# Optimization experiments

Measured on AMD Instinct MI355X. Metric: run time of the kernel, lower is better.

The kernel has to match this reference:

```python
import jax, jax.numpy as jnp
import numpy as np

N_NODES = 100000
N_EDGES = 3200000
NEG_SLOPE = 0.2  # PyG GATConv default


def _gat_conv(x, src, dst, W, a_src, a_dst, b, num_nodes):
    # x: [N, Fin]; src/dst: [E'] (self-loops already appended)
    h = x @ W                                   # [N, Fout]
    alpha_src = h @ a_src                       # [N]
    alpha_dst = h @ a_dst                       # [N]
    e = jax.nn.leaky_relu(alpha_src[src] + alpha_dst[dst], NEG_SLOPE)  # [E']
    # segment softmax over incoming edges of each destination node
    e_max = jax.ops.segment_max(e, dst, num_segments=num_nodes)
    e_exp = jnp.exp(e - e_max[dst])
    denom = jax.ops.segment_sum(e_exp, dst, num_segments=num_nodes)
    alpha = e_exp / (denom[dst] + 1e-16)        # [E']
    out = jax.ops.segment_sum(h[src] * alpha[:, None], dst, num_segments=num_nodes)
    return out + b


def setup_inputs() -> dict:
    key = jax.random.key(0)
    ks = jax.random.split(key, 10)
    x = jax.random.normal(ks[0], (N_NODES, 1), jnp.float32)
    edge_index = jax.random.randint(ks[1], (2, N_EDGES), 0, N_NODES, dtype=jnp.int64)
    s1 = 1.0  # glorot-ish scales
    return {
        "x": x,
        "edge_index": edge_index,
        "W1": jax.random.normal(ks[2], (1, 20), jnp.float32) * s1,
        "a_src1": jax.random.normal(ks[3], (20,), jnp.float32) * 0.3,
        "a_dst1": jax.random.normal(ks[4], (20,), jnp.float32) * 0.3,
        "b1": jnp.zeros((20,), jnp.float32),
        "W2": jax.random.normal(ks[5], (20, 20), jnp.float32) * (1.0 / np.sqrt(20.0)),
        "a_src2": jax.random.normal(ks[6], (20,), jnp.float32) * 0.3,
        "a_dst2": jax.random.normal(ks[7], (20,), jnp.float32) * 0.3,
        "b2": jnp.zeros((20,), jnp.float32),
        "Wl": jax.random.normal(ks[8], (20, 1), jnp.float32) * (1.0 / np.sqrt(20.0)),
        "bl": jnp.zeros((1,), jnp.float32),
    }


def reference(x, edge_index, W1, a_src1, a_dst1, b1, W2, a_src2, a_dst2, b2, Wl, bl):
    n = x.shape[0]
    loop = jnp.arange(n, dtype=edge_index.dtype)
    src = jnp.concatenate([edge_index[0], loop])  # add_self_loops=True
    dst = jnp.concatenate([edge_index[1], loop])
    h = _gat_conv(x, src, dst, W1, a_src1, a_dst1, b1, n)
    h = jax.nn.relu(h)
    h = _gat_conv(h, src, dst, W2, a_src2, a_dst2, b2, n)
    h = jax.nn.relu(h)
    return h @ Wl + bl  # [N, 1]
```

## Files before the change

### kernel.cpp

```cpp
#include <hip/hip_runtime.h>
#include <hip/hip_fp16.h>

#define FDIM 20
#define NSLOPE 0.2f
#define BSHIFT 7
#define BSIZE 128
#define BCAP 4800
#define MAXBUCK 800
#define PGRID 256
#define HSTRIDE 32
#define ABLK 512
#define ITMAX 13
#define CHCAP 12544
#define OFFSTRIDE 132

__device__ __forceinline__ float lrelu(float v) { return v > 0.f ? v : NSLOPE * v; }

__global__ void k_init(const float* __restrict__ x, const float* __restrict__ W1,
                       const float* __restrict__ a_src, const float* __restrict__ a_dst,
                       float2* __restrict__ PX, float* __restrict__ AD,
                       int* __restrict__ gcur, int N)
{
    int i = blockIdx.x * blockDim.x + threadIdx.x;
    if (i < MAXBUCK) gcur[i] = 0;
    if (i >= N) return;
    float cs = 0.f, cd = 0.f;
#pragma unroll
    for (int f = 0; f < FDIM; ++f) { float w = W1[f]; cs += w * a_src[f]; cd += w * a_dst[f]; }
    float xv = x[i];
    PX[i] = make_float2(xv * cs, xv);
    AD[i] = xv * cd;
}

__global__ void __launch_bounds__(1024)
k_part(const int* __restrict__ ei, int E, int nbuck,
       int* __restrict__ gcur, int* __restrict__ slab)
{
    __shared__ int hist[MAXBUCK];
    __shared__ int lofs[MAXBUCK];
    __shared__ int gbase[MAXBUCK];
    __shared__ int sbuf[CHCAP];
    __shared__ unsigned short sbk[CHCAP];
    const int tid = threadIdx.x;
    const int chunk = (E + PGRID - 1) / PGRID;
    const int c0 = blockIdx.x * chunk;
    const int c1 = min(c0 + chunk, E);
    for (int t = tid; t < nbuck; t += 1024) hist[t] = 0;
    __syncthreads();

    int ent[ITMAX], meta[ITMAX];
#pragma unroll
    for (int it = 0; it < ITMAX; ++it) {
        int i = c0 + tid + (it << 10);
        meta[it] = -1;
        if (i < c1) {
            int s = ei[i], d = ei[E + i];
            int b = d >> BSHIFT;
            int lp = atomicAdd(&hist[b], 1);
            ent[it]  = (s << BSHIFT) | (d & (BSIZE - 1));
            meta[it] = (lp << 10) | b;
        }
    }
    __syncthreads();

    int myc = 0;
    if (tid < nbuck) {
        myc = hist[tid];
        lofs[tid] = myc;
        gbase[tid] = myc ? atomicAdd(gcur + tid, myc) : 0;
    }
    __syncthreads();
    for (int o = 1; o < nbuck; o <<= 1) {
        int v = 0;
        if (tid < nbuck && tid >= o) v = lofs[tid - o];
        __syncthreads();
        if (tid < nbuck && tid >= o) lofs[tid] += v;
        __syncthreads();
    }
    if (tid < nbuck) lofs[tid] -= myc;
    __syncthreads();

#pragma unroll
    for (int it = 0; it < ITMAX; ++it) {
        int m = meta[it];
        if (m >= 0) {
            int b  = m & 1023;
            int lp = m >> 10;
            int pos = lofs[b] + lp;
            sbuf[pos] = ent[it];
            sbk[pos]  = (unsigned short)b;
        }
    }
    __syncthreads();

    const int cnt = c1 - c0;
    for (int i = tid; i < cnt; i += 1024) {
        int b  = sbk[i];
        int gp = gbase[b] + (i - lofs[b]);
        if (gp < BCAP) slab[(size_t)b * BCAP + gp] = sbuf[i];
    }
}

__device__ __forceinline__ void sort_bucket(const int* __restrict__ sp, int cnt,
                                            int* __restrict__ sedge,
                                            int* __restrict__ off,
                                            int* __restrict__ cur)
{
    const int tid = threadIdx.x;
    if (tid < BSIZE + 1) off[tid] = 0;
    __syncthreads();
    for (int i = tid; i < cnt; i += blockDim.x)
        atomicAdd(&off[(sp[i] & (BSIZE - 1)) + 1], 1);
    __syncthreads();
    for (int o = 1; o < BSIZE; o <<= 1) {
        int v = 0;
        if (tid < BSIZE && tid + 1 > o) v = off[tid + 1 - o];
        __syncthreads();
        if (tid < BSIZE) off[tid + 1] += v;
        __syncthreads();
    }
    if (tid < BSIZE) cur[tid] = off[tid];
    __syncthreads();
    for (int i = tid; i < cnt; i += blockDim.x) {
        int e = sp[i];
        int pos = atomicAdd(&cur[e & (BSIZE - 1)], 1);
        sedge[pos] = e >> BSHIFT;
    }
    __syncthreads();
}

__global__ void __launch_bounds__(ABLK)
k_agg1(const int* __restrict__ gcur, const int* __restrict__ slab,
       const float2* __restrict__ PX, const float* __restrict__ AD,
       const float* __restrict__ W1, const float* __restrict__ b1,
       const float* __restrict__ W2,
       const float* __restrict__ as2w, const float* __restrict__ ad2w,
       __half* __restrict__ H, float* __restrict__ AD2,
       int* __restrict__ sedge_g, int* __restrict__ off_g, int N)
{
    __shared__ int sedge[BCAP];
    __shared__ int off[BSIZE + 1], cur[BSIZE];
    __shared__ float sAD[BSIZE];
    __shared__ float sW1[FDIM], sb1[FDIM], sW2[FDIM * FDIM], sas[FDIM], sad[FDIM];
    const int tid = threadIdx.x;
    const int b = blockIdx.x;
    const int dbase = b << BSHIFT;
    if (tid < BSIZE) { int d = dbase + tid; sAD[tid] = (d < N) ? AD[d] : 0.f; }
    for (int t = tid; t < FDIM * FDIM; t += ABLK) sW2[t] = W2[t];
    if (tid >= 480 && tid < 480 + FDIM) {
        int k = tid - 480;
        sW1[k] = W1[k]; sb1[k] = b1[k]; sas[k] = as2w[k]; sad[k] = ad2w[k];
    }
    const int cnt = min(gcur[b], BCAP);
    sort_bucket(slab + (size_t)b * BCAP, cnt, sedge, off, cur);

    for (int i = tid; i < cnt; i += ABLK) sedge_g[(size_t)b * BCAP + i] = sedge[i];
    if (tid <= BSIZE) off_g[b * OFFSTRIDE + tid] = off[tid];

    const int dl = tid >> 2, sub = tid & 3;
    const float adv = sAD[dl];
    float den = 0.f, sx = 0.f;
    const int e1 = off[dl + 1];
#pragma unroll 2
    for (int j = off[dl] + sub; j < e1; j += 4) {
        int s = sedge[j];
        float2 p = PX[s];
        float w = __expf(lrelu(p.x + adv));
        den += w; sx += w * p.y;
    }
    den += __shfl_xor(den, 1); den += __shfl_xor(den, 2);
    sx  += __shfl_xor(sx, 1);  sx  += __shfl_xor(sx, 2);
    const int d = dbase + dl;
    if (sub == 0 && d < N) {
        float2 p = PX[d];
        float w = __expf(lrelu(p.x + adv));
        den += w; sx += w * p.y;
        float sv = sx / (den + 1e-16f);
        float tk[FDIM];
#pragma unroll
        for (int k = 0; k < FDIM; ++k) {
            float tv = sv * sW1[k] + sb1[k];
            tk[k] = tv > 0.f ? tv : 0.f;
        }
        float pas = 0.f, pad = 0.f;
        __half2* hrow = (__half2*)(H + (size_t)d * HSTRIDE);
#pragma unroll
        for (int f = 0; f < FDIM; f += 2) {
            float h0 = 0.f, h1 = 0.f;
#pragma unroll
            for (int k = 0; k < FDIM; ++k) {
                h0 += tk[k] * sW2[k * FDIM + f];
                h1 += tk[k] * sW2[k * FDIM + f + 1];
            }
            hrow[f >> 1] = __halves2half2(__float2half(h0), __float2half(h1));
            pas += h0 * sas[f] + h1 * sas[f + 1];
            pad += h0 * sad[f] + h1 * sad[f + 1];
        }
        *(float*)(H + (size_t)d * HSTRIDE + 24) = pas;
        AD2[d] = pad;
    }
}

__global__ void __launch_bounds__(ABLK)
k_agg2(const int* __restrict__ gcur, const int* __restrict__ sedge_g,
       const int* __restrict__ off_g,
       const __half* __restrict__ H, const float* __restrict__ AD2,
       const float* __restrict__ b2, const float* __restrict__ Wl,
       const float* __restrict__ bl,
       float* __restrict__ out, int N)
{
    __shared__ int sedge[BCAP];
    __shared__ int off[BSIZE + 1];
    __shared__ float sAD[BSIZE];
    __shared__ float sb2[FDIM], sWl[FDIM];
    const int tid = threadIdx.x;
    const int b = blockIdx.x;
    const int dbase = b << BSHIFT;
    if (tid < BSIZE) { int d = dbase + tid; sAD[tid] = (d < N) ? AD2[d] : 0.f; }
    if (tid >= 480 && tid < 480 + FDIM) {
        int k = tid - 480;
        sb2[k] = b2[k]; sWl[k] = Wl[k];
    }
    const int cnt = min(gcur[b], BCAP);
    for (int i = tid; i < cnt; i += ABLK) sedge[i] = sedge_g[(size_t)b * BCAP + i];
    if (tid <= BSIZE) off[tid] = off_g[b * OFFSTRIDE + tid];
    __syncthreads();

    const int dl = tid >> 2, sub = tid & 3;
    const int lane3 = (tid & 63) | 3;
    const float adv = sAD[dl];
    float den = 0.f;
    float acc[8];
#pragma unroll
    for (int t = 0; t < 8; ++t) acc[t] = 0.f;
    const int e1 = off[dl + 1];
#pragma unroll 2
    for (int j = off[dl]; j < e1; ++j) {
        int s = sedge[j];
        uint4 q = ((const uint4*)(H + (size_t)s * HSTRIDE))[sub];
        float al = __shfl(__uint_as_float(q.x), lane3);
        float w = __expf(lrelu(al + adv));
        den += w;
        float2 f;
        f = __half22float2(*(__half2*)&q.x); acc[0] += w * f.x; acc[1] += w * f.y;
        f = __half22float2(*(__half2*)&q.y); acc[2] += w * f.x; acc[3] += w * f.y;
        f = __half22float2(*(__half2*)&q.z); acc[4] += w * f.x; acc[5] += w * f.y;
        f = __half22float2(*(__half2*)&q.w); acc[6] += w * f.x; acc[7] += w * f.y;
    }

    const int d = dbase + dl;
    float r = 0.f;
    if (d < N) {
        uint4 q = ((const uint4*)(H + (size_t)d * HSTRIDE))[sub];
        float al = __shfl(__uint_as_float(q.x), lane3);
        float w = __expf(lrelu(al + adv));
        den += w;
        float hv[8];
        float2 f;
        f = __half22float2(*(__half2*)&q.x); hv[0] = f.x; hv[1] = f.y;
        f = __half22float2(*(__half2*)&q.y); hv[2] = f.x; hv[3] = f.y;
        f = __half22float2(*(__half2*)&q.z); hv[4] = f.x; hv[5] = f.y;
        f = __half22float2(*(__half2*)&q.w); hv[6] = f.x; hv[7] = f.y;
        float inv = 1.f / (den + 1e-16f);
        const int base = sub << 3;
        const int nf = (sub < 2) ? 8 : (sub == 2 ? 4 : 0);
#pragma unroll
        for (int t = 0; t < 8; ++t) {
            if (t < nf) {
                float v = (acc[t] + w * hv[t]) * inv + sb2[base + t];
                v = v > 0.f ? v : 0.f;
                r += v * sWl[base + t];
            }
        }
    }
    r += __shfl_xor(r, 1);
    r += __shfl_xor(r, 2);
    if (sub == 0 && d < N) out[d] = r + bl[0];
}

extern "C" void kernel_launch(void* const* d_in, const int* in_sizes, int n_in,
                              void* d_out, int out_size, void* d_ws, size_t ws_size,
                              hipStream_t stream)
{
    const float* x      = (const float*)d_in[0];
    const int*   ei     = (const int*)d_in[1];
    const float* W1     = (const float*)d_in[2];
    const float* a_src1 = (const float*)d_in[3];
    const float* a_dst1 = (const float*)d_in[4];
    const float* b1     = (const float*)d_in[5];
    const float* W2     = (const float*)d_in[6];
    const float* a_src2 = (const float*)d_in[7];
    const float* a_dst2 = (const float*)d_in[8];
    const float* b2     = (const float*)d_in[9];
    const float* Wl     = (const float*)d_in[10];
    const float* bl     = (const float*)d_in[11];
    float* out = (float*)d_out;

    const int N = in_sizes[0];
    const int E = in_sizes[1] / 2;
    const int NBUCK = (N + BSIZE - 1) >> BSHIFT;

    __half* H    = (__half*)d_ws;
    float2* PX   = (float2*)(H + (size_t)N * HSTRIDE);
    float*  AD   = (float*)(PX + N);
    float*  AD2  = AD + N;
    int*  gcur   = (int*)(AD2 + N);
    int*  slab   = gcur + MAXBUCK;
    int*  sedge_g = slab + (size_t)MAXBUCK * BCAP;
    int*  off_g   = sedge_g + (size_t)MAXBUCK * BCAP;

    const int nb_n = (N + 255) / 256;

    k_init<<<nb_n, 256, 0, stream>>>(x, W1, a_src1, a_dst1, PX, AD, gcur, N);
    k_part<<<PGRID, 1024, 0, stream>>>(ei, E, NBUCK, gcur, slab);
    k_agg1<<<NBUCK, ABLK, 0, stream>>>(gcur, slab, PX, AD, W1, b1, W2,
                                       a_src2, a_dst2, H, AD2, sedge_g, off_g, N);
    k_agg2<<<NBUCK, ABLK, 0, stream>>>(gcur, sedge_g, off_g, H, AD2, b2, Wl, bl, out, N);
}
```

Baseline: 181.8 us.

## Fuse both GAT aggregation layers into one persistent kernel with grid barrier

Merges the two aggregation kernels into a single persistent kernel of 512 blocks, each handling up to two buckets. The sorted edge lists, offsets and per-node layer-2 destination scores stay in shared memory across a software grid barrier, so the global sedge/off/AD2 round trip and one launch go away. The sort's block-level Hillis-Steele prefix scan is replaced by a single-wavefront shuffle scan. The grid barrier assumes all 512 blocks are co-resident, and the doubled shared-memory footprint (about 40KB per block) limits occupancy.

```diff
diff --git a/kernel.cpp b/kernel.cpp
--- a/kernel.cpp
+++ b/kernel.cpp
@@ -10,9 +10,9 @@
 #define PGRID 256
 #define HSTRIDE 32
 #define ABLK 512
+#define FGRID 512
 #define ITMAX 13
 #define CHCAP 12544
-#define OFFSTRIDE 132
 
 __device__ __forceinline__ float lrelu(float v) { return v > 0.f ? v : NSLOPE * v; }
 
@@ -22,7 +22,7 @@
                        int* __restrict__ gcur, int N)
 {
     int i = blockIdx.x * blockDim.x + threadIdx.x;
-    if (i < MAXBUCK) gcur[i] = 0;
+    if (i < MAXBUCK + 1) gcur[i] = 0;
     if (i >= N) return;
     float cs = 0.f, cd = 0.f;
 #pragma unroll
@@ -109,19 +109,27 @@
     const int tid = threadIdx.x;
     if (tid < BSIZE + 1) off[tid] = 0;
     __syncthreads();
-    for (int i = tid; i < cnt; i += blockDim.x)
+    for (int i = tid; i < cnt; i += ABLK)
         atomicAdd(&off[(sp[i] & (BSIZE - 1)) + 1], 1);
     __syncthreads();
-    for (int o = 1; o < BSIZE; o <<= 1) {
-        int v = 0;
-        if (tid < BSIZE && tid + 1 > o) v = off[tid + 1 - o];
-        __syncthreads();
-        if (tid < BSIZE) off[tid + 1] += v;
-        __syncthreads();
-    }
-    if (tid < BSIZE) cur[tid] = off[tid];
-    __syncthreads();
-    for (int i = tid; i < cnt; i += blockDim.x) {
+    if (tid < 64) {
+        int a = off[2 * tid + 1];
+        int c = off[2 * tid + 2];
+        int s = a + c;
+#pragma unroll
+        for (int o = 1; o < 64; o <<= 1) {
+            int t = __shfl_up(s, o);
+            if (tid >= o) s += t;
+        }
+        int ex = s - a - c;
+        off[2 * tid]     = ex;
+        off[2 * tid + 1] = ex + a;
+        cur[2 * tid]     = ex;
+        cur[2 * tid + 1] = ex + a;
+        if (tid == 63) off[BSIZE] = s;
+    }
+    __syncthreads();
+    for (int i = tid; i < cnt; i += ABLK) {
         int e = sp[i];
         int pos = atomicAdd(&cur[e & (BSIZE - 1)], 1);
         sedge[pos] = e >> BSHIFT;
@@ -129,153 +137,153 @@
     __syncthreads();
 }
 
-__global__ void __launch_bounds__(ABLK)
-k_agg1(const int* __restrict__ gcur, const int* __restrict__ slab,
-       const float2* __restrict__ PX, const float* __restrict__ AD,
-       const float* __restrict__ W1, const float* __restrict__ b1,
-       const float* __restrict__ W2,
-       const float* __restrict__ as2w, const float* __restrict__ ad2w,
-       __half* __restrict__ H, float* __restrict__ AD2,
-       int* __restrict__ sedge_g, int* __restrict__ off_g, int N)
-{
-    __shared__ int sedge[BCAP];
-    __shared__ int off[BSIZE + 1], cur[BSIZE];
-    __shared__ float sAD[BSIZE];
+__global__ void __launch_bounds__(ABLK, 4)
+k_fused(const int* __restrict__ gcur, const int* __restrict__ slab,
+        const float2* __restrict__ PX, const float* __restrict__ AD,
+        const float* __restrict__ W1, const float* __restrict__ b1,
+        const float* __restrict__ W2,
+        const float* __restrict__ as2w, const float* __restrict__ ad2w,
+        const float* __restrict__ b2, const float* __restrict__ Wl,
+        const float* __restrict__ bl,
+        __half* __restrict__ H, float* __restrict__ out,
+        int* __restrict__ bar, int N, int nbuck)
+{
+    __shared__ int sedge[2][BCAP];
+    __shared__ int off[2][BSIZE + 1];
+    __shared__ int cur[BSIZE];
+    __shared__ float sADv[2][BSIZE];
+    __shared__ float sAD2[2][BSIZE];
     __shared__ float sW1[FDIM], sb1[FDIM], sW2[FDIM * FDIM], sas[FDIM], sad[FDIM];
+    __shared__ float sb2[FDIM], sWl[FDIM];
     const int tid = threadIdx.x;
-    const int b = blockIdx.x;
-    const int dbase = b << BSHIFT;
-    if (tid < BSIZE) { int d = dbase + tid; sAD[tid] = (d < N) ? AD[d] : 0.f; }
+
     for (int t = tid; t < FDIM * FDIM; t += ABLK) sW2[t] = W2[t];
     if (tid >= 480 && tid < 480 + FDIM) {
         int k = tid - 480;
         sW1[k] = W1[k]; sb1[k] = b1[k]; sas[k] = as2w[k]; sad[k] = ad2w[k];
     }
-    const int cnt = min(gcur[b], BCAP);
-    sort_bucket(slab + (size_t)b * BCAP, cnt, sedge, off, cur);
-
-    for (int i = tid; i < cnt; i += ABLK) sedge_g[(size_t)b * BCAP + i] = sedge[i];
-    if (tid <= BSIZE) off_g[b * OFFSTRIDE + tid] = off[tid];
-
-    const int dl = tid >> 2, sub = tid & 3;
-    const float adv = sAD[dl];
-    float den = 0.f, sx = 0.f;
-    const int e1 = off[dl + 1];
+    if (tid >= 448 && tid < 448 + FDIM) {
+        int k = tid - 448;
+        sb2[k] = b2[k]; sWl[k] = Wl[k];
+    }
+
+    for (int h = 0; h < 2; ++h) {
+        const int b = blockIdx.x + (h << 9);
+        if (b >= nbuck) break;
+        const int dbase = b << BSHIFT;
+        if (tid < BSIZE) { int d = dbase + tid; sADv[h][tid] = (d < N) ? AD[d] : 0.f; }
+        const int cnt = min(gcur[b], BCAP);
+        sort_bucket(slab + (size_t)b * BCAP, cnt, sedge[h], off[h], cur);
+
+        const int dl = tid >> 2, sub = tid & 3;
+        const float adv = sADv[h][dl];
+        float den = 0.f, sx = 0.f;
+        const int e1 = off[h][dl + 1];
 #pragma unroll 2
-    for (int j = off[dl] + sub; j < e1; j += 4) {
-        int s = sedge[j];
-        float2 p = PX[s];
-        float w = __expf(lrelu(p.x + adv));
-        den += w; sx += w * p.y;
-    }
-    den += __shfl_xor(den, 1); den += __shfl_xor(den, 2);
-    sx  += __shfl_xor(sx, 1);  sx  += __shfl_xor(sx, 2);
-    const int d = dbase + dl;
-    if (sub == 0 && d < N) {
-        float2 p = PX[d];
-        float w = __expf(lrelu(p.x + adv));
-        den += w; sx += w * p.y;
-        float sv = sx / (den + 1e-16f);
-        float tk[FDIM];
-#pragma unroll
-        for (int k = 0; k < FDIM; ++k) {
-            float tv = sv * sW1[k] + sb1[k];
-            tk[k] = tv > 0.f ? tv : 0.f;
-        }
-        float pas = 0.f, pad = 0.f;
-        __half2* hrow = (__half2*)(H + (size_t)d * HSTRIDE);
-#pragma unroll
-        for (int f = 0; f < FDIM; f += 2) {
-            float h0 = 0.f, h1 = 0.f;
+        for (int j = off[h][dl] + sub; j < e1; j += 4) {
+            int s = sedge[h][j];
+            float2 p = PX[s];
+            float w = __expf(lrelu(p.x + adv));
+            den += w; sx += w * p.y;
+        }
+        den += __shfl_xor(den, 1); den += __shfl_xor(den, 2);
+        sx  += __shfl_xor(sx, 1);  sx  += __shfl_xor(sx, 2);
+        const int d = dbase + dl;
+        if (sub == 0 && d < N) {
+            float2 p = PX[d];
+            float w = __expf(lrelu(p.x + adv));
+            den += w; sx += w * p.y;
+            float sv = sx / (den + 1e-16f);
+            float tk[FDIM];
 #pragma unroll
             for (int k = 0; k < FDIM; ++k) {
-                h0 += tk[k] * sW2[k * FDIM + f];
-                h1 += tk[k] * sW2[k * FDIM + f + 1];
+                float tv = sv * sW1[k] + sb1[k];
+                tk[k] = tv > 0.f ? tv : 0.f;
             }
-            hrow[f >> 1] = __halves2half2(__float2half(h0), __float2half(h1));
-            pas += h0 * sas[f] + h1 * sas[f + 1];
-            pad += h0 * sad[f] + h1 * sad[f + 1];
-        }
-        *(float*)(H + (size_t)d * HSTRIDE + 24) = pas;
-        AD2[d] = pad;
-    }
-}
-
-__global__ void __launch_bounds__(ABLK)
-k_agg2(const int* __restrict__ gcur, const int* __restrict__ sedge_g,
-       const int* __restrict__ off_g,
-       const __half* __restrict__ H, const float* __restrict__ AD2,
-       const float* __restrict__ b2, const float* __restrict__ Wl,
-       const float* __restrict__ bl,
-       float* __restrict__ out, int N)
-{
-    __shared__ int sedge[BCAP];
-    __shared__ int off[BSIZE + 1];
-    __shared__ float sAD[BSIZE];
-    __shared__ float sb2[FDIM], sWl[FDIM];
-    const int tid = threadIdx.x;
-    const int b = blockIdx.x;
-    const int dbase = b << BSHIFT;
-    if (tid < BSIZE) { int d = dbase + tid; sAD[tid] = (d < N) ? AD2[d] : 0.f; }
-    if (tid >= 480 && tid < 480 + FDIM) {
-        int k = tid - 480;
-        sb2[k] = b2[k]; sWl[k] = Wl[k];
-    }
-    const int cnt = min(gcur[b], BCAP);
-    for (int i = tid; i < cnt; i += ABLK) sedge[i] = sedge_g[(size_t)b * BCAP + i];
-    if (tid <= BSIZE) off[tid] = off_g[b * OFFSTRIDE + tid];
-    __syncthreads();
-
-    const int dl = tid >> 2, sub = tid & 3;
-    const int lane3 = (tid & 63) | 3;
-    const float adv = sAD[dl];
-    float den = 0.f;
-    float acc[8];
-#pragma unroll
-    for (int t = 0; t < 8; ++t) acc[t] = 0.f;
-    const int e1 = off[dl + 1];
+            float pas = 0.f, pad = 0.f;
+            __half2* hrow = (__half2*)(H + (size_t)d * HSTRIDE);
+#pragma unroll
+            for (int f = 0; f < FDIM; f += 2) {
+                float h0 = 0.f, h1 = 0.f;
+#pragma unroll
+                for (int k = 0; k < FDIM; ++k) {
+                    h0 += tk[k] * sW2[k * FDIM + f];
+                    h1 += tk[k] * sW2[k * FDIM + f + 1];
+                }
+                hrow[f >> 1] = __halves2half2(__float2half(h0), __float2half(h1));
+                pas += h0 * sas[f] + h1 * sas[f + 1];
+                pad += h0 * sad[f] + h1 * sad[f + 1];
+            }
+            *(float*)(H + (size_t)d * HSTRIDE + 24) = pas;
+            sAD2[h][dl] = pad;
+        }
+    }
+
+    __threadfence();
+    __syncthreads();
+    if (tid == 0) {
+        atomicAdd(bar, 1);
+        while (__hip_atomic_load(bar, __ATOMIC_ACQUIRE, __HIP_MEMORY_SCOPE_AGENT)
+               < (int)gridDim.x)
+            __builtin_amdgcn_s_sleep(2);
+    }
+    __syncthreads();
+    __threadfence();
+
+    for (int h = 0; h < 2; ++h) {
+        const int b = blockIdx.x + (h << 9);
+        if (b >= nbuck) break;
+        const int dbase = b << BSHIFT;
+        const int dl = tid >> 2, sub = tid & 3;
+        const int lane3 = (tid & 63) | 3;
+        const float adv = sAD2[h][dl];
+        float den = 0.f;
+        float acc[8];
+#pragma unroll
+        for (int t = 0; t < 8; ++t) acc[t] = 0.f;
+        const int e1 = off[h][dl + 1];
 #pragma unroll 2
-    for (int j = off[dl]; j < e1; ++j) {
-        int s = sedge[j];
-        uint4 q = ((const uint4*)(H + (size_t)s * HSTRIDE))[sub];
-        float al = __shfl(__uint_as_float(q.x), lane3);
-        float w = __expf(lrelu(al + adv));
-        den += w;
-        float2 f;
-        f = __half22float2(*(__half2*)&q.x); acc[0] += w * f.x; acc[1] += w * f.y;
-        f = __half22float2(*(__half2*)&q.y); acc[2] += w * f.x; acc[3] += w * f.y;
-        f = __half22float2(*(__half2*)&q.z); acc[4] += w * f.x; acc[5] += w * f.y;
-        f = __half22float2(*(__half2*)&q.w); acc[6] += w * f.x; acc[7] += w * f.y;
-    }
-
-    const int d = dbase + dl;
-    float r = 0.f;
-    if (d < N) {
-        uint4 q = ((const uint4*)(H + (size_t)d * HSTRIDE))[sub];
-        float al = __shfl(__uint_as_float(q.x), lane3);
-        float w = __expf(lrelu(al + adv));
-        den += w;
-        float hv[8];
-        float2 f;
-        f = __half22float2(*(__half2*)&q.x); hv[0] = f.x; hv[1] = f.y;
-        f = __half22float2(*(__half2*)&q.y); hv[2] = f.x; hv[3] = f.y;
-        f = __half22float2(*(__half2*)&q.z); hv[4] = f.x; hv[5] = f.y;
-        f = __half22float2(*(__half2*)&q.w); hv[6] = f.x; hv[7] = f.y;
-        float inv = 1.f / (den + 1e-16f);
-        const int base = sub << 3;
-        const int nf = (sub < 2) ? 8 : (sub == 2 ? 4 : 0);
-#pragma unroll
-        for (int t = 0; t < 8; ++t) {
-            if (t < nf) {
-                float v = (acc[t] + w * hv[t]) * inv + sb2[base + t];
-                v = v > 0.f ? v : 0.f;
-                r += v * sWl[base + t];
+        for (int j = off[h][dl]; j < e1; ++j) {
+            int s = sedge[h][j];
+            uint4 q = ((const uint4*)(H + (size_t)s * HSTRIDE))[sub];
+            float al = __shfl(__uint_as_float(q.x), lane3);
+            float w = __expf(lrelu(al + adv));
+            den += w;
+            float2 f;
+            f = __half22float2(*(__half2*)&q.x); acc[0] += w * f.x; acc[1] += w * f.y;
+            f = __half22float2(*(__half2*)&q.y); acc[2] += w * f.x; acc[3] += w * f.y;
+            f = __half22float2(*(__half2*)&q.z); acc[4] += w * f.x; acc[5] += w * f.y;
+            f = __half22float2(*(__half2*)&q.w); acc[6] += w * f.x; acc[7] += w * f.y;
+        }
+        const int d = dbase + dl;
+        float r = 0.f;
+        if (d < N) {
+            uint4 q = ((const uint4*)(H + (size_t)d * HSTRIDE))[sub];
+            float al = __shfl(__uint_as_float(q.x), lane3);
+            float w = __expf(lrelu(al + adv));
+            den += w;
+            float hv[8];
+            float2 f;
+            f = __half22float2(*(__half2*)&q.x); hv[0] = f.x; hv[1] = f.y;
+            f = __half22float2(*(__half2*)&q.y); hv[2] = f.x; hv[3] = f.y;
+            f = __half22float2(*(__half2*)&q.z); hv[4] = f.x; hv[5] = f.y;
+            f = __half22float2(*(__half2*)&q.w); hv[6] = f.x; hv[7] = f.y;
+            float inv = 1.f / (den + 1e-16f);
+            const int base = sub << 3;
+            const int nf = (sub < 2) ? 8 : (sub == 2 ? 4 : 0);
+#pragma unroll
+            for (int t = 0; t < 8; ++t) {
+                if (t < nf) {
+                    float v = (acc[t] + w * hv[t]) * inv + sb2[base + t];
+                    v = v > 0.f ? v : 0.f;
+                    r += v * sWl[base + t];
+                }
             }
         }
-    }
-    r += __shfl_xor(r, 1);
-    r += __shfl_xor(r, 2);
-    if (sub == 0 && d < N) out[d] = r + bl[0];
+        r += __shfl_xor(r, 1);
+        r += __shfl_xor(r, 2);
+        if (sub == 0 && d < N) out[d] = r + bl[0];
+    }
 }
 
 extern "C" void kernel_launch(void* const* d_in, const int* in_sizes, int n_in,
@@ -300,20 +308,18 @@
     const int E = in_sizes[1] / 2;
     const int NBUCK = (N + BSIZE - 1) >> BSHIFT;
 
-    __half* H    = (__half*)d_ws;
-    float2* PX   = (float2*)(H + (size_t)N * HSTRIDE);
-    float*  AD   = (float*)(PX + N);
-    float*  AD2  = AD + N;
-    int*  gcur   = (int*)(AD2 + N);
-    int*  slab   = gcur + MAXBUCK;
-    int*  sedge_g = slab + (size_t)MAXBUCK * BCAP;
-    int*  off_g   = sedge_g + (size_t)MAXBUCK * BCAP;
+    __half* H   = (__half*)d_ws;
+    float2* PX  = (float2*)(H + (size_t)N * HSTRIDE);
+    float*  AD  = (float*)(PX + N);
+    int*  gcur  = (int*)(AD + N);
+    int*  bar   = gcur + MAXBUCK;
+    int*  slab  = gcur + MAXBUCK + 1;
 
     const int nb_n = (N + 255) / 256;
 
     k_init<<<nb_n, 256, 0, stream>>>(x, W1, a_src1, a_dst1, PX, AD, gcur, N);
     k_part<<<PGRID, 1024, 0, stream>>>(ei, E, NBUCK, gcur, slab);
-    k_agg1<<<NBUCK, ABLK, 0, stream>>>(gcur, slab, PX, AD, W1, b1, W2,
-                                       a_src2, a_dst2, H, AD2, sedge_g, off_g, N);
-    k_agg2<<<NBUCK, ABLK, 0, stream>>>(gcur, sedge_g, off_g, H, AD2, b2, Wl, bl, out, N);
-}
+    k_fused<<<FGRID, ABLK, 0, stream>>>(gcur, slab, PX, AD, W1, b1, W2,
+                                        a_src2, a_dst2, b2, Wl, bl,
+                                        H, out, bar, N, NBUCK);
+}
```

New measurement: 464.9 us. 156% more time.

## Fuse node init into partition kernel, double partition grid, warp-shuffle bucket scan

Applied to the files above, without the earlier changes.

Folds the per-node init computation (PX/AD) into the edge partition kernel and replaces the gcur zeroing with a memset, removing one kernel launch. The partition grid doubles to 512 blocks with a halved per-block chunk and shared buffer, which raises parallelism and may improve occupancy. The bucket-sort prefix scan now uses a single-wavefront shuffle scan instead of a log-step barrier loop. The fused init only covers all nodes if 512*1024 >= N, which holds here, and the memset still adds a separate stream operation.

```diff
diff --git a/kernel.cpp b/kernel.cpp
--- a/kernel.cpp
+++ b/kernel.cpp
@@ -7,34 +7,21 @@
 #define BSIZE 128
 #define BCAP 4800
 #define MAXBUCK 800
-#define PGRID 256
+#define PGRID 512
 #define HSTRIDE 32
 #define ABLK 512
-#define ITMAX 13
-#define CHCAP 12544
+#define ITMAX 7
+#define CHCAP 6272
 #define OFFSTRIDE 132
 
 __device__ __forceinline__ float lrelu(float v) { return v > 0.f ? v : NSLOPE * v; }
-
-__global__ void k_init(const float* __restrict__ x, const float* __restrict__ W1,
-                       const float* __restrict__ a_src, const float* __restrict__ a_dst,
-                       float2* __restrict__ PX, float* __restrict__ AD,
-                       int* __restrict__ gcur, int N)
-{
-    int i = blockIdx.x * blockDim.x + threadIdx.x;
-    if (i < MAXBUCK) gcur[i] = 0;
-    if (i >= N) return;
-    float cs = 0.f, cd = 0.f;
-#pragma unroll
-    for (int f = 0; f < FDIM; ++f) { float w = W1[f]; cs += w * a_src[f]; cd += w * a_dst[f]; }
-    float xv = x[i];
-    PX[i] = make_float2(xv * cs, xv);
-    AD[i] = xv * cd;
-}
 
 __global__ void __launch_bounds__(1024)
 k_part(const int* __restrict__ ei, int E, int nbuck,
-       int* __restrict__ gcur, int* __restrict__ slab)
+       const float* __restrict__ x, const float* __restrict__ W1,
+       const float* __restrict__ a_src, const float* __restrict__ a_dst,
+       float2* __restrict__ PX, float* __restrict__ AD,
+       int* __restrict__ gcur, int* __restrict__ slab, int N)
 {
     __shared__ int hist[MAXBUCK];
     __shared__ int lofs[MAXBUCK];
@@ -42,6 +29,21 @@
     __shared__ int sbuf[CHCAP];
     __shared__ unsigned short sbk[CHCAP];
     const int tid = threadIdx.x;
+
+    {
+        int g = blockIdx.x * 1024 + tid;
+        if (g < N) {
+            float cs = 0.f, cd = 0.f;
+#pragma unroll
+            for (int f = 0; f < FDIM; ++f) {
+                float w = W1[f]; cs += w * a_src[f]; cd += w * a_dst[f];
+            }
+            float xv = x[g];
+            PX[g] = make_float2(xv * cs, xv);
+            AD[g] = xv * cd;
+        }
+    }
+
     const int chunk = (E + PGRID - 1) / PGRID;
     const int c0 = blockIdx.x * chunk;
     const int c1 = min(c0 + chunk, E);
@@ -109,19 +111,27 @@
     const int tid = threadIdx.x;
     if (tid < BSIZE + 1) off[tid] = 0;
     __syncthreads();
-    for (int i = tid; i < cnt; i += blockDim.x)
+    for (int i = tid; i < cnt; i += ABLK)
         atomicAdd(&off[(sp[i] & (BSIZE - 1)) + 1], 1);
     __syncthreads();
-    for (int o = 1; o < BSIZE; o <<= 1) {
-        int v = 0;
-        if (tid < BSIZE && tid + 1 > o) v = off[tid + 1 - o];
-        __syncthreads();
-        if (tid < BSIZE) off[tid + 1] += v;
-        __syncthreads();
-    }
-    if (tid < BSIZE) cur[tid] = off[tid];
-    __syncthreads();
-    for (int i = tid; i < cnt; i += blockDim.x) {
+    if (tid < 64) {
+        int a = off[2 * tid + 1];
+        int c = off[2 * tid + 2];
+        int s = a + c;
+#pragma unroll
+        for (int o = 1; o < 64; o <<= 1) {
+            int t = __shfl_up(s, o);
+            if (tid >= o) s += t;
+        }
+        int ex = s - a - c;
+        off[2 * tid]     = ex;
+        off[2 * tid + 1] = ex + a;
+        cur[2 * tid]     = ex;
+        cur[2 * tid + 1] = ex + a;
+        if (tid == 63) off[BSIZE] = s;
+    }
+    __syncthreads();
+    for (int i = tid; i < cnt; i += ABLK) {
         int e = sp[i];
         int pos = atomicAdd(&cur[e & (BSIZE - 1)], 1);
         sedge[pos] = e >> BSHIFT;
@@ -309,10 +319,9 @@
     int*  sedge_g = slab + (size_t)MAXBUCK * BCAP;
     int*  off_g   = sedge_g + (size_t)MAXBUCK * BCAP;
 
-    const int nb_n = (N + 255) / 256;
-
-    k_init<<<nb_n, 256, 0, stream>>>(x, W1, a_src1, a_dst1, PX, AD, gcur, N);
-    k_part<<<PGRID, 1024, 0, stream>>>(ei, E, NBUCK, gcur, slab);
+    hipMemsetAsync(gcur, 0, MAXBUCK * sizeof(int), stream);
+    k_part<<<PGRID, 1024, 0, stream>>>(ei, E, NBUCK, x, W1, a_src1, a_dst1,
+                                       PX, AD, gcur, slab, N);
     k_agg1<<<NBUCK, ABLK, 0, stream>>>(gcur, slab, PX, AD, W1, b1, W2,
                                        a_src2, a_dst2, H, AD2, sedge_g, off_g, N);
     k_agg2<<<NBUCK, ABLK, 0, stream>>>(gcur, sedge_g, off_g, H, AD2, b2, Wl, bl, out, N);
```

After: 183.8 us. About the same (+1.1%).
